# Kernel tuning notes

Hardware: AMD Instinct MI355X
Metric: run time of the kernel (lower is better)

## Reference

```python
import jax, jax.numpy as jnp
import numpy as np

TEMPERATURE = 0.1
EPS = 1e-12  # torch F.normalize eps


def setup_inputs() -> dict:
    key = jax.random.key(0)
    k1, k2 = jax.random.split(key)
    B, D = 4096, 512
    z_i = jax.random.normal(k1, (B, D), dtype=jnp.float32)
    z_j = jax.random.normal(k2, (B, D), dtype=jnp.float32)
    return {"z_i": z_i, "z_j": z_j}


def reference(z_i, z_j):
    B = z_i.shape[0]
    N = 2 * B
    z = jnp.concatenate([z_i, z_j], axis=0)  # [N, D]
    norm = jnp.linalg.norm(z, axis=1, keepdims=True)
    z = z / jnp.maximum(norm, EPS)
    sim = jnp.matmul(z, z.T) / TEMPERATURE  # [N, N]

    idx = jnp.arange(N)
    neg_inf = jnp.float32(-jnp.inf)
    # mask self-similarity diagonal
    sim = sim.at[idx, idx].set(neg_inf)

    b = jnp.arange(B)
    # positives: diag(sim, +B) then diag(sim, -B)
    positives = jnp.concatenate([sim[b, b + B], sim[b + B, b]]).reshape(N, 1)

    # negatives: sim with positive pairs also masked to -inf
    negatives = sim.at[b, b + B].set(neg_inf)
    negatives = negatives.at[b + B, b].set(neg_inf)

    logits = jnp.concatenate([positives, negatives], axis=1)  # [N, N+1]
    # cross entropy with target class 0 for every row
    lse = jax.scipy.special.logsumexp(logits, axis=1)
    loss = jnp.mean(lse - logits[:, 0])
    return loss
```

## Files before the change

kernel.cpp:

```cpp
#include <hip/hip_runtime.h>
#include <hip/hip_bf16.h>

#define BATCH 4096
#define NTOT  8192
#define DIM   512
#define NBLK  2080

typedef __attribute__((ext_vector_type(4))) float floatx4;
typedef __attribute__((ext_vector_type(8))) int   intx8;

#define ASYNC16(gp, lp)                                                        \
  __builtin_amdgcn_global_load_lds(                                            \
      (__attribute__((address_space(1))) void*)(gp),                           \
      (__attribute__((address_space(3))) void*)(lp), 16, 0, 0)

__device__ __forceinline__ unsigned q4(float v) {
  const float m = fabsf(v);
  int c;
  if      (m < 0.25f) c = 0;
  else if (m < 0.75f) c = 1;
  else if (m < 1.25f) c = 2;
  else if (m < 1.75f) c = 3;
  else if (m < 2.50f) c = 4;
  else if (m < 3.50f) c = 5;
  else if (m < 5.00f) c = 6;
  else                c = 7;
  return (unsigned)(c | (v < 0.0f ? 8 : 0));
}

__global__ __launch_bounds__(256) void nrm_kernel(const float* __restrict__ zi,
                                                  const float* __restrict__ zj,
                                                  unsigned char* __restrict__ zn,
                                                  float* __restrict__ S,
                                                  float* __restrict__ out) {
  if (blockIdx.x < 32) S[blockIdx.x * 256 + threadIdx.x] = 0.0f;
  if (blockIdx.x == 32 && threadIdx.x == 0) out[0] = 0.0f;
  const int row = blockIdx.x * 4 + (threadIdx.x >> 6);
  const int l   = threadIdx.x & 63;
  const float* src = (row < BATCH) ? (zi + (size_t)row * DIM)
                                   : (zj + (size_t)(row - BATCH) * DIM);
  const float4* s4 = (const float4*)src;
  float4 v0 = s4[l];
  float4 v1 = s4[l + 64];
  float ss = v0.x*v0.x + v0.y*v0.y + v0.z*v0.z + v0.w*v0.w
           + v1.x*v1.x + v1.y*v1.y + v1.z*v1.z + v1.w*v1.w;
  #pragma unroll
  for (int m = 1; m < 64; m <<= 1) ss += __shfl_xor(ss, m, 64);
  const float r = 64.0f / fmaxf(sqrtf(ss), 1e-12f);
  unsigned short p0 = (unsigned short)(q4(v0.x * r) | (q4(v0.y * r) << 4)
                     | (q4(v0.z * r) << 8) | (q4(v0.w * r) << 12));
  unsigned short p1 = (unsigned short)(q4(v1.x * r) | (q4(v1.y * r) << 4)
                     | (q4(v1.z * r) << 8) | (q4(v1.w * r) << 12));
  unsigned short* d = (unsigned short*)(zn + (size_t)row * 256);
  d[l]      = p0;
  d[l + 64] = p1;
}

__global__ __launch_bounds__(256) void simsum_kernel(const unsigned char* __restrict__ zn,
                                                     float* __restrict__ S,
                                                     float* __restrict__ P) {
  const int u = blockIdx.x;
  int bj = (int)((sqrtf(8.0f * (float)u + 1.0f) - 1.0f) * 0.5f);
  while ((bj + 1) * (bj + 2) / 2 <= u) ++bj;
  while (bj * (bj + 1) / 2 > u) --bj;
  const int bi = u - bj * (bj + 1) / 2;
  const bool diag = (bi == bj);
  const bool posb = (bj == bi + BATCH / 128);

  __shared__ __align__(16) unsigned char shA[2 * 8192];
  __shared__ __align__(16) unsigned char shB[2 * 8192];
  __shared__ float redR[2][128];
  __shared__ float redC[2][128];

  const int t    = threadIdx.x;
  const int w    = t >> 6;
  const int l    = t & 63;
  const int quad = l >> 4;
  const int lo   = l & 15;
  const int wm   = w >> 1;
  const int wn   = w & 1;
  const int tileRow = bi * 128;
  const int tileCol = bj * 128;

  const int rr   = t >> 2;
  const int koff = ((t & 3) ^ (rr & 3) ^ ((rr >> 2) & 3)) * 16;
  const unsigned char* gA0 = zn + (size_t)(tileRow + rr     ) * 256 + koff;
  const unsigned char* gA1 = zn + (size_t)(tileRow + rr + 64) * 256 + koff;
  const unsigned char* gB0 = zn + (size_t)(tileCol + rr     ) * 256 + koff;
  const unsigned char* gB1 = zn + (size_t)(tileCol + rr + 64) * 256 + koff;
  unsigned char* lA0 = shA + w * 1024;
  unsigned char* lA1 = shA + w * 1024 + 4096;
  unsigned char* lB0 = shB + w * 1024;
  unsigned char* lB1 = shB + w * 1024 + 4096;

  floatx4 acc[4][4];
  #pragma unroll
  for (int i = 0; i < 4; ++i)
    #pragma unroll
    for (int j = 0; j < 4; ++j)
      acc[i][j] = (floatx4){0.f, 0.f, 0.f, 0.f};

  const int sw   = (quad ^ (lo & 3) ^ ((lo >> 2) & 3)) * 16;
  const int aRow = (wm * 64 + lo) * 64 + sw;
  const int bRow = (wn * 64 + lo) * 64 + sw;

  #define STAGE(bufo)                                                         \
    ASYNC16(gA0, lA0 + (bufo)); ASYNC16(gA1, lA1 + (bufo));                   \
    ASYNC16(gB0, lB0 + (bufo)); ASYNC16(gB1, lB1 + (bufo));                   \
    gA0 += 64; gA1 += 64; gB0 += 64; gB1 += 64;

  STAGE(0)

  #pragma unroll
  for (int it = 0; it < 4; ++it) {
    __syncthreads();
    const int co = (it & 1) * 8192;
    const int no = co ^ 8192;
    if (it < 3) { STAGE(no) }
    union frag { int4 h[2]; intx8 v; };
    frag aF[4], bF[4];
    #pragma unroll
    for (int i = 0; i < 4; ++i) {
      aF[i].h[0] = *(const int4*)(shA + co + aRow + i * 1024);
      aF[i].h[1] = aF[i].h[0];
    }
    #pragma unroll
    for (int j = 0; j < 4; ++j) {
      bF[j].h[0] = *(const int4*)(shB + co + bRow + j * 1024);
      bF[j].h[1] = bF[j].h[0];
    }
    #pragma unroll
    for (int i = 0; i < 4; ++i)
      #pragma unroll
      for (int j = 0; j < 4; ++j)
        acc[i][j] = __builtin_amdgcn_mfma_scale_f32_16x16x128_f8f6f4(
            aF[i].v, bF[j].v, acc[i][j], 4, 4, 0, 127, 0, 127);
  }
  #undef STAGE

  const float LS = 10.0f / 4096.0f;
  float rs[4][4];
  float cs[4];
  #pragma unroll
  for (int i = 0; i < 4; ++i)
    #pragma unroll
    for (int r = 0; r < 4; ++r) rs[i][r] = 0.f;
  #pragma unroll
  for (int j = 0; j < 4; ++j) cs[j] = 0.f;

  #pragma unroll
  for (int i = 0; i < 4; ++i)
    #pragma unroll
    for (int j = 0; j < 4; ++j)
      #pragma unroll
      for (int r = 0; r < 4; ++r) {
        const float e = __expf(acc[i][j][r] * LS - 10.0f);
        rs[i][r] += e;
        cs[j] += e;
      }

  if (wm == wn && quad == (lo >> 2)) {
    const int r = lo & 3;
    if (diag) {
      #pragma unroll
      for (int i = 0; i < 4; ++i) {
        const float e = __expf(acc[i][i][r] * LS - 10.0f);
        rs[i][r] -= e;
        cs[i] -= e;
      }
    }
    if (posb) {
      #pragma unroll
      for (int i = 0; i < 4; ++i) {
        const int row = tileRow + wm * 64 + i * 16 + lo;
        const float v = acc[i][i][r] * LS;
        P[row] = v;
        P[row + BATCH] = v;
      }
    }
  }

  #pragma unroll
  for (int m = 1; m < 16; m <<= 1) {
    #pragma unroll
    for (int i = 0; i < 4; ++i)
      #pragma unroll
      for (int r = 0; r < 4; ++r)
        rs[i][r] += __shfl_xor(rs[i][r], m, 64);
  }
  if (lo == 0) {
    #pragma unroll
    for (int i = 0; i < 4; ++i)
      #pragma unroll
      for (int r = 0; r < 4; ++r)
        redR[wn][wm * 64 + i * 16 + quad * 4 + r] = rs[i][r];
  }
  #pragma unroll
  for (int m = 16; m < 64; m <<= 1) {
    #pragma unroll
    for (int j = 0; j < 4; ++j) cs[j] += __shfl_xor(cs[j], m, 64);
  }
  if (quad == 0) {
    #pragma unroll
    for (int j = 0; j < 4; ++j)
      redC[wm][wn * 64 + j * 16 + lo] = cs[j];
  }
  __syncthreads();
  if (t < 128) {
    atomicAdd(&S[tileRow + t], redR[0][t] + redR[1][t]);
  } else if (!diag) {
    const int c = t - 128;
    atomicAdd(&S[tileCol + c], redC[0][c] + redC[1][c]);
  }
}

__global__ __launch_bounds__(256) void loss_kernel(const float* __restrict__ S,
                                                   const float* __restrict__ P,
                                                   float* __restrict__ out) {
  const int i = blockIdx.x * 256 + threadIdx.x;
  float a = 10.0f + logf(S[i]) - P[i];
  #pragma unroll
  for (int m = 1; m < 64; m <<= 1) a += __shfl_xor(a, m, 64);
  __shared__ float sb[4];
  if ((threadIdx.x & 63) == 0) sb[threadIdx.x >> 6] = a;
  __syncthreads();
  if (threadIdx.x == 0)
    atomicAdd(out, (sb[0] + sb[1] + sb[2] + sb[3]) * (1.0f / (float)NTOT));
}

extern "C" void kernel_launch(void* const* d_in, const int* in_sizes, int n_in,
                              void* d_out, int out_size, void* d_ws, size_t ws_size,
                              hipStream_t stream) {
  const float* zi = (const float*)d_in[0];
  const float* zj = (const float*)d_in[1];
  unsigned char* zn = (unsigned char*)d_ws;
  float*  S  = (float*)((char*)d_ws + (size_t)NTOT * DIM * 2);
  float*  P  = S + NTOT;
  float*  out = (float*)d_out;

  nrm_kernel<<<NTOT / 4, 256, 0, stream>>>(zi, zj, zn, S, out);
  simsum_kernel<<<NBLK, 256, 0, stream>>>(zn, S, P);
  loss_kernel<<<NTOT / 256, 256, 0, stream>>>(S, P, out);
}
```

Measured before the change: 90.06 us.

## Load whole K extent into LDS at once instead of double-buffered staging

Replaces the four-step double-buffered pipeline with a single bulk async load of the full 128x256-byte A and B tiles into LDS, then one barrier and four MFMA steps. This removes three barriers per block and the interleaving of issue and compute, and uses a new XOR swizzle over 16 chunks per row. In exchange LDS per block rises from 32KB to 64KB, which can reduce occupancy, and there is no longer any overlap between loading and compute within a block.

```diff
diff --git a/kernel.cpp b/kernel.cpp
--- a/kernel.cpp
+++ b/kernel.cpp
@@ -67,8 +67,8 @@
   const bool diag = (bi == bj);
   const bool posb = (bj == bi + BATCH / 128);
 
-  __shared__ __align__(16) unsigned char shA[2 * 8192];
-  __shared__ __align__(16) unsigned char shB[2 * 8192];
+  __shared__ __align__(16) unsigned char shA[32768];
+  __shared__ __align__(16) unsigned char shB[32768];
   __shared__ float redR[2][128];
   __shared__ float redC[2][128];
 
@@ -82,16 +82,15 @@
   const int tileRow = bi * 128;
   const int tileCol = bj * 128;
 
-  const int rr   = t >> 2;
-  const int koff = ((t & 3) ^ (rr & 3) ^ ((rr >> 2) & 3)) * 16;
-  const unsigned char* gA0 = zn + (size_t)(tileRow + rr     ) * 256 + koff;
-  const unsigned char* gA1 = zn + (size_t)(tileRow + rr + 64) * 256 + koff;
-  const unsigned char* gB0 = zn + (size_t)(tileCol + rr     ) * 256 + koff;
-  const unsigned char* gB1 = zn + (size_t)(tileCol + rr + 64) * 256 + koff;
-  unsigned char* lA0 = shA + w * 1024;
-  unsigned char* lA1 = shA + w * 1024 + 4096;
-  unsigned char* lB0 = shB + w * 1024;
-  unsigned char* lB1 = shB + w * 1024 + 4096;
+  const int rr   = t >> 4;
+  const int koff = ((t & 15) ^ rr) * 16;
+  #pragma unroll
+  for (int m = 0; m < 8; ++m) {
+    ASYNC16(zn + (size_t)(tileRow + rr + 16 * m) * 256 + koff,
+            shA + w * 1024 + m * 4096);
+    ASYNC16(zn + (size_t)(tileCol + rr + 16 * m) * 256 + koff,
+            shB + w * 1024 + m * 4096);
+  }
 
   floatx4 acc[4][4];
   #pragma unroll
@@ -100,33 +99,24 @@
     for (int j = 0; j < 4; ++j)
       acc[i][j] = (floatx4){0.f, 0.f, 0.f, 0.f};
 
-  const int sw   = (quad ^ (lo & 3) ^ ((lo >> 2) & 3)) * 16;
-  const int aRow = (wm * 64 + lo) * 64 + sw;
-  const int bRow = (wn * 64 + lo) * 64 + sw;
-
-  #define STAGE(bufo)                                                         \
-    ASYNC16(gA0, lA0 + (bufo)); ASYNC16(gA1, lA1 + (bufo));                   \
-    ASYNC16(gB0, lB0 + (bufo)); ASYNC16(gB1, lB1 + (bufo));                   \
-    gA0 += 64; gA1 += 64; gB0 += 64; gB1 += 64;
-
-  STAGE(0)
-
-  #pragma unroll
-  for (int it = 0; it < 4; ++it) {
-    __syncthreads();
-    const int co = (it & 1) * 8192;
-    const int no = co ^ 8192;
-    if (it < 3) { STAGE(no) }
+  const int aBase = (wm * 64 + lo) * 256;
+  const int bBase = (wn * 64 + lo) * 256;
+
+  __syncthreads();
+
+  #pragma unroll
+  for (int kk = 0; kk < 4; ++kk) {
+    const int sw = ((kk * 4 + quad) ^ lo) * 16;
     union frag { int4 h[2]; intx8 v; };
     frag aF[4], bF[4];
     #pragma unroll
     for (int i = 0; i < 4; ++i) {
-      aF[i].h[0] = *(const int4*)(shA + co + aRow + i * 1024);
+      aF[i].h[0] = *(const int4*)(shA + aBase + i * 4096 + sw);
       aF[i].h[1] = aF[i].h[0];
     }
     #pragma unroll
     for (int j = 0; j < 4; ++j) {
-      bF[j].h[0] = *(const int4*)(shB + co + bRow + j * 1024);
+      bF[j].h[0] = *(const int4*)(shB + bBase + j * 4096 + sw);
       bF[j].h[1] = bF[j].h[0];
     }
     #pragma unroll
@@ -136,7 +126,6 @@
         acc[i][j] = __builtin_amdgcn_mfma_scale_f32_16x16x128_f8f6f4(
             aF[i].v, bF[j].v, acc[i][j], 4, 4, 0, 127, 0, 127);
   }
-  #undef STAGE
 
   const float LS = 10.0f / 4096.0f;
   float rs[4][4];
```

Measured after the change: 92.54 us. 1.03x slower.
